# Kernel tuning notes

Hardware: AMD Instinct MI355X
Metric: run time of the kernel (lower is better)

The kernel has to match this reference:

```python
import jax, jax.numpy as jnp
import numpy as np

PHI = 0.1  # fraction of pruned weights randomized per inference


def setup_inputs() -> dict:
    key = jax.random.key(0)
    k1, k2, k3 = jax.random.split(key, 3)
    d_out, d_in, batch = 8192, 8192, 256
    W = jax.random.normal(k1, (d_out, d_in), jnp.float32) * 0.02
    prune = jax.random.uniform(k2, (d_out, d_in)) < 0.9
    W = jnp.where(prune, 0.0, W)
    mask = (W == 0.0)  # _register_masks: pruned positions
    x = jax.random.normal(k3, (batch, d_in), jnp.float32)
    return {"x": x, "W": W, "mask": mask}


def reference(x, W, mask):
    # --- _apply_random_flip (vectorized) ---
    n_pruned = int(np.asarray(jnp.sum(mask)))          # concrete mask -> static count
    n_flip = max(1, int(PHI * n_pruned))
    keep = ~mask
    n_keep = jnp.sum(keep).astype(W.dtype)
    wk = jnp.where(keep, W, 0.0)
    mean = jnp.sum(wk) / n_keep
    # torch .std() is unbiased (n-1 denominator)
    var = jnp.sum(jnp.where(keep, (W - mean) ** 2, 0.0)) / (n_keep - 1.0)
    std = jnp.sqrt(var)
    key = jax.random.key(42)
    ks, kv = jax.random.split(key)
    # uniform random permutation of pruned indices -> top_k of random scores
    scores = jnp.where(mask.ravel(), jax.random.uniform(ks, (W.size,)), -1.0)
    _, flip_idx = jax.lax.top_k(scores, n_flip)        # [n_flip] flat indices into W
    vals = jax.random.normal(kv, (n_flip,), W.dtype) * std * 0.1
    W_flipped = W.ravel().at[flip_idx].set(vals).reshape(W.shape)
    # --- base_model forward (Linear, no bias) ---
    out = x @ W_flipped.T                               # [batch, d_out]
    # --- _restore_masks: zero flipped weights again (no effect on out) ---
    _ = jnp.where(mask, 0.0, W_flipped)
    return out
```

## Files before the change

### kernel.cpp

```cpp
#include <hip/hip_runtime.h>

typedef unsigned int u32;
typedef unsigned long long u64;
typedef unsigned short u16;

#define NTOT   67108864u
#define T0P    7399424u
#define PBASE  14452u
#define NSUP   1932u
#define NWSEG  4096u
#define WCAP   2176u
#define RCAP   4352u
#define KSPLIT 4

struct Scalars {
  double sumW;
  double sumW2;
  u64 npruned;
  u64 nflip;
  float stdf;
  float pad;
};

#define OFF_COLSUM 0ull
#define OFF_ALLOC  8192ull
#define OFF_SBASE  16384ull
#define OFF_SC     24576ull
#define OFF_SEGCNT 24704ull
#define OFF_BHIST  41216ull
#define OFF_BDEST  2138368ull
#define OFF_XBF    4235520ull
#define OFF_SEGS   8429824ull
#define OFF_ROUTED 44081408ull

__host__ __device__ inline void tf2x32(u32 k0, u32 k1, u32 x0, u32 x1, u32& y0, u32& y1) {
  u32 ks2 = k0 ^ k1 ^ 0x1BD11BDAu;
  x0 += k0; x1 += k1;
#define TFR(r) { x0 += x1; x1 = (x1 << (r)) | (x1 >> (32 - (r))); x1 ^= x0; }
  TFR(13) TFR(15) TFR(26) TFR(6)  x0 += k1;  x1 += ks2 + 1u;
  TFR(17) TFR(29) TFR(16) TFR(24) x0 += ks2; x1 += k0 + 2u;
  TFR(13) TFR(15) TFR(26) TFR(6)  x0 += k0;  x1 += k1 + 3u;
  TFR(17) TFR(29) TFR(16) TFR(24) x0 += k1;  x1 += ks2 + 4u;
  TFR(13) TFR(15) TFR(26) TFR(6)  x0 += ks2; x1 += k0 + 5u;
#undef TFR
  y0 = x0; y1 = x1;
}

__device__ inline u32 jax_bits32(u32 k0, u32 k1, u32 i) {
  u32 y0, y1; tf2x32(k0, k1, 0u, i, y0, y1);
  return y0 ^ y1;
}

__device__ inline u16 f2bf(float f) {
  union { float f; u32 u; } c; c.f = f;
  u32 r = ((c.u >> 16) & 1u) + 0x7FFFu;
  return (u16)((c.u + r) >> 16);
}

__device__ inline float erfinv32(float x) {
  float w = -log1pf(-x * x);
  float p;
  if (w < 5.0f) {
    w -= 2.5f;
    p = 2.81022636e-08f;
    p = fmaf(p, w, 3.43273939e-07f);
    p = fmaf(p, w, -3.5233877e-06f);
    p = fmaf(p, w, -4.39150654e-06f);
    p = fmaf(p, w, 0.00021858087f);
    p = fmaf(p, w, -0.00125372503f);
    p = fmaf(p, w, -0.00417768164f);
    p = fmaf(p, w, 0.246640727f);
    p = fmaf(p, w, 1.50140941f);
  } else {
    w = sqrtf(w) - 3.0f;
    p = -0.000200214257f;
    p = fmaf(p, w, 0.000100950558f);
    p = fmaf(p, w, 0.00134934322f);
    p = fmaf(p, w, -0.00367342844f);
    p = fmaf(p, w, 0.00573950773f);
    p = fmaf(p, w, -0.0076224613f);
    p = fmaf(p, w, 0.00943887047f);
    p = fmaf(p, w, 1.00167406f);
    p = fmaf(p, w, 2.83297682f);
  }
  return p * x;
}

__global__ __launch_bounds__(256) void k_pass1(const float* __restrict__ W, Scalars* sc,
                                               u32* segcnt, u32* segs, u32 uk0, u32 uk1) {
  u32 t = threadIdx.x;
  u32 gid = blockIdx.x * 256 + t;
  u32 lane = t & 63;
  u32 wid = gid >> 6;
  u32* wseg = segs + (u64)wid * WCAP;
  u32 wbase = 0;
  double s = 0.0, s2 = 0.0; u32 cnt = 0;
  const u32 stride4 = 1024u * 256u * 4u;
  for (u32 b4 = gid * 4; b4 < NTOT; b4 += stride4) {
    float4 w4 = *(const float4*)(W + b4);
    u32 sb0 = jax_bits32(uk0, uk1, b4 + 0) >> 9;
    u32 sb1 = jax_bits32(uk0, uk1, b4 + 1) >> 9;
    u32 sb2 = jax_bits32(uk0, uk1, b4 + 2) >> 9;
    u32 sb3 = jax_bits32(uk0, uk1, b4 + 3) >> 9;
    float we[4] = {w4.x, w4.y, w4.z, w4.w};
    u32 sbv[4] = {sb0, sb1, sb2, sb3};
    u32 cand[4]; u32 nc = 0;
#pragma unroll
    for (int e = 0; e < 4; e++) {
      float w = we[e];
      s  += (double)w;
      s2 += (double)w * (double)w;
      bool pr = (w == 0.0f);
      cnt += pr ? 1u : 0u;
      if (pr && sbv[e] >= T0P) { cand[nc] = b4 + e; nc++; }
    }
    u32 inc = nc;
#pragma unroll
    for (int o = 1; o < 64; o <<= 1) { u32 v = (u32)__shfl_up((int)inc, o); if (lane >= (u32)o) inc += v; }
    u32 tot = (u32)__shfl((int)inc, 63);
    u32 pos = wbase + inc - nc;
    for (u32 k2 = 0; k2 < nc; k2++)
      if (pos + k2 < WCAP) wseg[pos + k2] = cand[k2];
    wbase += tot;
  }
  for (int o = 32; o > 0; o >>= 1) {
    s += __shfl_down(s, o); s2 += __shfl_down(s2, o); cnt += __shfl_down(cnt, o);
  }
  if (lane == 0) {
    atomicAdd(&sc->sumW, s);
    atomicAdd(&sc->sumW2, s2);
    atomicAdd(&sc->npruned, (u64)cnt);
    segcnt[wid] = (wbase > WCAP) ? WCAP : wbase;
  }
}

__global__ __launch_bounds__(256) void k_route_a(const u32* __restrict__ segs,
                                                 const u32* __restrict__ segcnt,
                                                 u32* bhist, u32 uk0, u32 uk1) {
  __shared__ u32 lhist[2048];
  u32 t = threadIdx.x;
  for (u32 j = t; j < 2048; j += 256) lhist[j] = 0;
  __syncthreads();
#pragma unroll 1
  for (int sg = 0; sg < 16; sg++) {
    u32 wid = blockIdx.x * 16 + sg;
    u32 n = segcnt[wid]; if (n > WCAP) n = WCAP;
    const u32* sp = segs + (u64)wid * WCAP;
    for (u32 i = t; i < n; i += 256) {
      u32 sup = (jax_bits32(uk0, uk1, sp[i]) >> 18) - PBASE;
      atomicAdd(&lhist[sup], 1u);
    }
  }
  __syncthreads();
  for (u32 j = t; j < 2048; j += 256) bhist[blockIdx.x * 2048 + j] = lhist[j];
}

__global__ __launch_bounds__(256) void k_colscan(const u32* __restrict__ bhist,
                                                 u32* bdest, u32* colsum) {
  __shared__ u32 wtmp[4];
  u32 s = blockIdx.x, t = threadIdx.x, lane = t & 63, wv = t >> 6;
  u32 v = bhist[t * 2048 + s];
  u32 inc = v;
#pragma unroll
  for (int o = 1; o < 64; o <<= 1) { u32 x = (u32)__shfl_up((int)inc, o); if (lane >= (u32)o) inc += x; }
  if (lane == 63) wtmp[wv] = inc;
  __syncthreads();
  u32 woff = 0;
  for (u32 w = 0; w < wv; w++) woff += wtmp[w];
  bdest[t * 2048 + s] = woff + inc - v;
  if (t == 255) colsum[s] = woff + inc;
}

__global__ __launch_bounds__(256) void k_scan(const u32* __restrict__ colsum, Scalars* sc,
                                              u32* alloc, u32* sbase) {
  __shared__ u32 h[2048];
  __shared__ u32 wtmp[4];
  u32 t = threadIdx.x, lane = t & 63, wv = t >> 6;
  for (u32 j = t; j < 2048; j += 256) h[j] = colsum[j];
  __syncthreads();
  {
    u32 a[8]; u32 s8 = 0;
#pragma unroll
    for (int k = 0; k < 8; k++) { a[k] = h[t * 8 + k]; s8 += a[k]; }
    u32 inc = s8;
#pragma unroll
    for (int o = 1; o < 64; o <<= 1) { u32 v = (u32)__shfl_up((int)inc, o); if (lane >= (u32)o) inc += v; }
    if (lane == 63) wtmp[wv] = inc;
    __syncthreads();
    u32 woff = 0; for (u32 w = 0; w < wv; w++) woff += wtmp[w];
    u32 base = woff + inc - s8;
#pragma unroll
    for (int k = 0; k < 8; k++) { alloc[t * 8 + k] = base; base += a[k]; }
    __syncthreads();
  }
  {
    u32 a[8]; u32 s8 = 0;
#pragma unroll
    for (int k = 0; k < 8; k++) { a[k] = h[2047 - (t * 8 + k)]; s8 += a[k]; }
    u32 inc = s8;
#pragma unroll
    for (int o = 1; o < 64; o <<= 1) { u32 v = (u32)__shfl_up((int)inc, o); if (lane >= (u32)o) inc += v; }
    if (lane == 63) wtmp[wv] = inc;
    __syncthreads();
    u32 woff = 0; for (u32 w = 0; w < wv; w++) woff += wtmp[w];
    u32 base = woff + inc - s8;
#pragma unroll
    for (int k = 0; k < 8; k++) { sbase[2047 - (t * 8 + k)] = base; base += a[k]; }
  }
  if (t == 0) {
    double nk = (double)NTOT - (double)sc->npruned;
    double mean = sc->sumW / nk;
    double var = (sc->sumW2 - 2.0 * mean * sc->sumW + nk * mean * mean) / (nk - 1.0);
    sc->stdf = (float)sqrt(var);
    u64 nfi = (u64)(0.1 * (double)sc->npruned);
    if (nfi < 1) nfi = 1;
    sc->nflip = nfi;
  }
}

__global__ __launch_bounds__(256) void k_route_b(const u32* __restrict__ segs,
                                                 const u32* __restrict__ segcnt,
                                                 const u32* __restrict__ alloc,
                                                 const u32* __restrict__ bdest,
                                                 u32* routed, u32 uk0, u32 uk1) {
  __shared__ u32 lcur[2048];
  u32 t = threadIdx.x;
  for (u32 j = t; j < 2048; j += 256) lcur[j] = alloc[j] + bdest[blockIdx.x * 2048 + j];
  __syncthreads();
#pragma unroll 1
  for (int sg = 0; sg < 16; sg++) {
    u32 wid = blockIdx.x * 16 + sg;
    u32 n = segcnt[wid]; if (n > WCAP) n = WCAP;
    const u32* sp = segs + (u64)wid * WCAP;
    for (u32 i = t; i < n; i += 256) {
      u32 idx = sp[i];
      u32 sup = (jax_bits32(uk0, uk1, idx) >> 18) - PBASE;
      u32 pos = atomicAdd(&lcur[sup], 1u);
      routed[pos] = idx;
    }
  }
}

__device__ inline void suf512(const u32* cnt, u32* suf, u32* wtmp) {
  u32 t = threadIdx.x, lane = t & 63, wv = t >> 6;
  u32 a0 = cnt[511 - t * 2], a1 = cnt[510 - t * 2];
  u32 s = a0 + a1;
  u32 inc = s;
#pragma unroll
  for (int o = 1; o < 64; o <<= 1) { u32 v = (u32)__shfl_up((int)inc, o); if (lane >= (u32)o) inc += v; }
  if (lane == 63) wtmp[wv] = inc;
  __syncthreads();
  u32 woff = 0;
  for (u32 w = 0; w < wv; w++) woff += wtmp[w];
  u32 base = woff + inc - s;
  suf[511 - t * 2] = base;
  suf[510 - t * 2] = base + a0;
  __syncthreads();
}

__global__ __launch_bounds__(256) void k_rank(float* __restrict__ W,
                                              const u32* __restrict__ colsum,
                                              const u32* __restrict__ alloc,
                                              const u32* __restrict__ sbase,
                                              const u32* __restrict__ routed,
                                              const Scalars* __restrict__ sc,
                                              u32 uk0, u32 uk1, u32 vk0, u32 vk1) {
  u32 p = blockIdx.x;
  u32 n = colsum[p]; if (n == 0) return;
  if (n > RCAP) n = RCAP;
  u64 nflip = sc->nflip;
  u32 rbase = sbase[p];
  if ((u64)rbase >= nflip) return;
  __shared__ u32 sIdx[RCAP];
  __shared__ u16 sFine[RCAP];
  __shared__ u32 pIdx[RCAP];
  __shared__ u32 hist[512], gbase[512], cur[512], wtmp[4];
  u32 t = threadIdx.x;
  for (u32 j = t; j < 512; j += 256) hist[j] = 0;
  __syncthreads();
  const u32* src = routed + alloc[p];
  for (u32 i = t; i < n; i += 256) {
    u32 idx = src[i];
    u32 f = (jax_bits32(uk0, uk1, idx) >> 9) & 511u;
    sIdx[i] = idx;
    sFine[i] = (u16)f;
    atomicAdd(&hist[f], 1u);
  }
  __syncthreads();
  suf512(hist, gbase, wtmp);
  for (u32 j = t; j < 512; j += 256) cur[j] = gbase[j];
  __syncthreads();
  for (u32 i = t; i < n; i += 256) {
    u32 pos = atomicAdd(&cur[sFine[i]], 1u);
    pIdx[pos] = sIdx[i];
  }
  __syncthreads();
  float stdf = sc->stdf;
  for (u32 i = t; i < n; i += 256) {
    u32 f = sFine[i];
    u32 g0 = gbase[f], g1 = g0 + hist[f];
    u32 v = sIdx[i];
    u32 ord = 0;
    for (u32 q = g0; q < g1; q++) ord += (pIdx[q] < v) ? 1u : 0u;
    u64 rank = (u64)rbase + g0 + ord;
    if (rank >= nflip) continue;
    u32 bits = jax_bits32(vk0, vk1, (u32)rank);
    union { u32 u; float fl; } cv; cv.u = 0x3F800000u | (bits >> 9);
    float fu = cv.fl - 1.0f;
    const float lo = -0.99999994f;
    float u2 = fmaxf(lo, fu * 2.0f + lo);
    float nrm = 1.41421354f * erfinv32(u2);
    W[v] = (nrm * stdf) * 0.1f;
  }
}

__global__ __launch_bounds__(256) void k_xconv(const float* __restrict__ x, u16* __restrict__ xbf) {
  u32 i = blockIdx.x * blockDim.x + threadIdx.x;
  float4 v = ((const float4*)x)[i];
  ushort4 o; o.x = f2bf(v.x); o.y = f2bf(v.y); o.z = f2bf(v.z); o.w = f2bf(v.w);
  ((ushort4*)xbf)[i] = o;
}

typedef __bf16 bf16x8 __attribute__((ext_vector_type(8)));
typedef float f32x4 __attribute__((ext_vector_type(4)));

__global__ __launch_bounds__(256, 2) void k_gemm(const u16* __restrict__ xbf,
                                                 const float* __restrict__ W,
                                                 float* __restrict__ out) {
  __shared__ u16 xs[256 * 72];
  __shared__ u16 wsm[64 * 72];
  u32 tid = threadIdx.x;
  u32 lane = tid & 63, wv = tid >> 6;
  u32 nt0 = blockIdx.x * 64;
  u32 kbase = blockIdx.y * (8192 / KSPLIT);
  f32x4 acc[4][4];
#pragma unroll
  for (int i = 0; i < 4; i++)
#pragma unroll
    for (int j = 0; j < 4; j++) acc[i][j] = (f32x4){0.f, 0.f, 0.f, 0.f};

  for (u32 kb = kbase; kb < kbase + 2048u; kb += 64u) {
#pragma unroll
    for (int r8 = 0; r8 < 8; r8++) {
      u32 row = r8 * 32 + (tid >> 3);
      u32 kseg = (tid & 7) * 8;
      uint4 v = *(const uint4*)(xbf + (u64)row * 8192 + kb + kseg);
      *(uint4*)&xs[row * 72 + kseg] = v;
    }
#pragma unroll
    for (int r = 0; r < 4; r++) {
      u32 f4 = r * 256 + tid;
      u32 row = f4 >> 4;
      u32 kc = (f4 & 15) * 4;
      float4 v = *(const float4*)(W + (u64)(nt0 + row) * 8192 + kb + kc);
      ushort4 o; o.x = f2bf(v.x); o.y = f2bf(v.y); o.z = f2bf(v.z); o.w = f2bf(v.w);
      *(ushort4*)&wsm[row * 72 + kc] = o;
    }
    __syncthreads();
#pragma unroll
    for (int ks = 0; ks < 2; ks++) {
      bf16x8 a[4], b[4];
      u32 koff = ks * 32 + (lane >> 4) * 8;
      u32 rsel = lane & 15;
#pragma unroll
      for (int mt = 0; mt < 4; mt++) a[mt] = *(bf16x8*)&xs[(wv * 64 + mt * 16 + rsel) * 72 + koff];
#pragma unroll
      for (int nt = 0; nt < 4; nt++) b[nt] = *(bf16x8*)&wsm[(nt * 16 + rsel) * 72 + koff];
#pragma unroll
      for (int mt = 0; mt < 4; mt++)
#pragma unroll
        for (int nt = 0; nt < 4; nt++)
          acc[mt][nt] = __builtin_amdgcn_mfma_f32_16x16x32_bf16(a[mt], b[nt], acc[mt][nt], 0, 0, 0);
    }
    __syncthreads();
  }
  u32 quad = lane >> 4, col = lane & 15;
#pragma unroll
  for (int mt = 0; mt < 4; mt++)
#pragma unroll
    for (int nt = 0; nt < 4; nt++) {
      u32 n = nt0 + nt * 16 + col;
#pragma unroll
      for (int rg = 0; rg < 4; rg++) {
        u32 m = wv * 64 + mt * 16 + quad * 4 + rg;
        atomicAdd(&out[(u64)m * 8192 + n], acc[mt][nt][rg]);
      }
    }
}

extern "C" void kernel_launch(void* const* d_in, const int* in_sizes, int n_in,
                              void* d_out, int out_size, void* d_ws, size_t ws_size,
                              hipStream_t stream) {
  const float* x; float* W;
  if (in_sizes[0] == 2097152) { x = (const float*)d_in[0]; W = (float*)d_in[1]; }
  else                        { x = (const float*)d_in[1]; W = (float*)d_in[0]; }
  float* out = (float*)d_out;
  char* ws = (char*)d_ws;

  u32* colsum = (u32*)(ws + OFF_COLSUM);
  u32* alloc  = (u32*)(ws + OFF_ALLOC);
  u32* sbase  = (u32*)(ws + OFF_SBASE);
  Scalars* sc = (Scalars*)(ws + OFF_SC);
  u32* segcnt = (u32*)(ws + OFF_SEGCNT);
  u32* bhist  = (u32*)(ws + OFF_BHIST);
  u32* bdest  = (u32*)(ws + OFF_BDEST);
  u16* xbf    = (u16*)(ws + OFF_XBF);
  u32* segs   = (u32*)(ws + OFF_SEGS);
  u32* routed = (u32*)(ws + OFF_ROUTED);

  u32 a0, a1, b0, b1;
  tf2x32(0u, 42u, 0u, 0u, a0, a1);
  tf2x32(0u, 42u, 0u, 1u, b0, b1);

  hipMemsetAsync(sc, 0, sizeof(Scalars), stream);
  hipMemsetAsync(out, 0, (size_t)out_size * 4, stream);

  k_xconv<<<2048, 256, 0, stream>>>(x, xbf);
  k_pass1<<<1024, 256, 0, stream>>>(W, sc, segcnt, segs, a0, a1);
  k_route_a<<<256, 256, 0, stream>>>(segs, segcnt, bhist, a0, a1);
  k_colscan<<<2048, 256, 0, stream>>>(bhist, bdest, colsum);
  k_scan<<<1, 256, 0, stream>>>(colsum, sc, alloc, sbase);
  k_route_b<<<256, 256, 0, stream>>>(segs, segcnt, alloc, bdest, routed, a0, a1);
  k_rank<<<NSUP, 256, 0, stream>>>(W, colsum, alloc, sbase, routed, sc, a0, a1, b0, b1);
  dim3 g(128, KSPLIT);
  k_gemm<<<g, 256, 0, stream>>>(xbf, W, out);
}
```

Measured before the change: 1.022 ms.

## Fuse histogram into pass1, prestage W as bf16, stop mutating input W

Pass1 now also writes a bf16 copy of W and builds the per-block superbucket histogram in shared memory, which removes the separate route_a kernel and its recomputation of random bits. The rank kernel writes flipped values into the bf16 copy, so the input W is no longer modified, and the GEMM loads bf16 W directly, halving its W traffic and dropping per-tile conversions. Histograms and offsets are stored as u16 with 8 histogram rows per colscan thread. The cost is an extra 128MB bf16 write in pass1, and the u16 counts could overflow if candidate counts were larger.

```diff
diff --git a/kernel.cpp b/kernel.cpp
--- a/kernel.cpp
+++ b/kernel.cpp
@@ -8,8 +8,9 @@
 #define T0P    7399424u
 #define PBASE  14452u
 #define NSUP   1932u
-#define NWSEG  4096u
-#define WCAP   2176u
+#define NBLK   2048u
+#define NWSEG  8192u
+#define WCAP   1152u
 #define RCAP   4352u
 #define KSPLIT 4
 
@@ -26,12 +27,13 @@
 #define OFF_ALLOC  8192ull
 #define OFF_SBASE  16384ull
 #define OFF_SC     24576ull
-#define OFF_SEGCNT 24704ull
-#define OFF_BHIST  41216ull
-#define OFF_BDEST  2138368ull
-#define OFF_XBF    4235520ull
-#define OFF_SEGS   8429824ull
-#define OFF_ROUTED 44081408ull
+#define OFF_SEGCNT 24832ull
+#define OFF_BHIST  57600ull
+#define OFF_BDEST  8446208ull
+#define OFF_XBF    16834816ull
+#define OFF_WBF    21029120ull
+#define OFF_SEGS   155246848ull
+#define OFF_ROUTED 192995584ull
 
 __host__ __device__ inline void tf2x32(u32 k0, u32 k1, u32 x0, u32 x1, u32& y0, u32& y1) {
   u32 ks2 = k0 ^ k1 ^ 0x1BD11BDAu;
@@ -87,7 +89,11 @@
 }
 
 __global__ __launch_bounds__(256) void k_pass1(const float* __restrict__ W, Scalars* sc,
-                                               u32* segcnt, u32* segs, u32 uk0, u32 uk1) {
+                                               u32* segcnt, u32* segs, u16* bhist,
+                                               u16* wbf, u32 uk0, u32 uk1) {
+  __shared__ u32 lhist[2048];
+  for (u32 j = threadIdx.x; j < 2048; j += 256) lhist[j] = 0;
+  __syncthreads();
   u32 t = threadIdx.x;
   u32 gid = blockIdx.x * 256 + t;
   u32 lane = t & 63;
@@ -95,24 +101,29 @@
   u32* wseg = segs + (u64)wid * WCAP;
   u32 wbase = 0;
   double s = 0.0, s2 = 0.0; u32 cnt = 0;
-  const u32 stride4 = 1024u * 256u * 4u;
-  for (u32 b4 = gid * 4; b4 < NTOT; b4 += stride4) {
-    float4 w4 = *(const float4*)(W + b4);
-    u32 sb0 = jax_bits32(uk0, uk1, b4 + 0) >> 9;
-    u32 sb1 = jax_bits32(uk0, uk1, b4 + 1) >> 9;
-    u32 sb2 = jax_bits32(uk0, uk1, b4 + 2) >> 9;
-    u32 sb3 = jax_bits32(uk0, uk1, b4 + 3) >> 9;
-    float we[4] = {w4.x, w4.y, w4.z, w4.w};
-    u32 sbv[4] = {sb0, sb1, sb2, sb3};
-    u32 cand[4]; u32 nc = 0;
-#pragma unroll
-    for (int e = 0; e < 4; e++) {
-      float w = we[e];
-      s  += (double)w;
-      s2 += (double)w * (double)w;
-      bool pr = (w == 0.0f);
+  const u32 stride8 = NBLK * 256u * 8u;
+  for (u32 b8 = gid * 8; b8 < NTOT; b8 += stride8) {
+    float4 wa = *(const float4*)(W + b8);
+    float4 wb = *(const float4*)(W + b8 + 4);
+    u32 sb[8];
+#pragma unroll
+    for (int e = 0; e < 8; e++) sb[e] = jax_bits32(uk0, uk1, b8 + e) >> 9;
+    float we[8] = {wa.x, wa.y, wa.z, wa.w, wb.x, wb.y, wb.z, wb.w};
+    ushort4 o1, o2;
+    o1.x = f2bf(wa.x); o1.y = f2bf(wa.y); o1.z = f2bf(wa.z); o1.w = f2bf(wa.w);
+    o2.x = f2bf(wb.x); o2.y = f2bf(wb.y); o2.z = f2bf(wb.z); o2.w = f2bf(wb.w);
+    *(ushort4*)(wbf + b8) = o1;
+    *(ushort4*)(wbf + b8 + 4) = o2;
+    float cs  = ((wa.x + wa.y) + (wa.z + wa.w)) + ((wb.x + wb.y) + (wb.z + wb.w));
+    float cs2 = ((wa.x * wa.x + wa.y * wa.y) + (wa.z * wa.z + wa.w * wa.w)) +
+                ((wb.x * wb.x + wb.y * wb.y) + (wb.z * wb.z + wb.w * wb.w));
+    s += (double)cs; s2 += (double)cs2;
+    u32 candI[8], candS[8]; u32 nc = 0;
+#pragma unroll
+    for (int e = 0; e < 8; e++) {
+      bool pr = (we[e] == 0.0f);
       cnt += pr ? 1u : 0u;
-      if (pr && sbv[e] >= T0P) { cand[nc] = b4 + e; nc++; }
+      if (pr && sb[e] >= T0P) { candI[nc] = b8 + e; candS[nc] = (sb[e] >> 9) - PBASE; nc++; }
     }
     u32 inc = nc;
 #pragma unroll
@@ -120,7 +131,7 @@
     u32 tot = (u32)__shfl((int)inc, 63);
     u32 pos = wbase + inc - nc;
     for (u32 k2 = 0; k2 < nc; k2++)
-      if (pos + k2 < WCAP) wseg[pos + k2] = cand[k2];
+      if (pos + k2 < WCAP) { wseg[pos + k2] = candI[k2]; atomicAdd(&lhist[candS[k2]], 1u); }
     wbase += tot;
   }
   for (int o = 32; o > 0; o >>= 1) {
@@ -132,43 +143,28 @@
     atomicAdd(&sc->npruned, (u64)cnt);
     segcnt[wid] = (wbase > WCAP) ? WCAP : wbase;
   }
-}
-
-__global__ __launch_bounds__(256) void k_route_a(const u32* __restrict__ segs,
-                                                 const u32* __restrict__ segcnt,
-                                                 u32* bhist, u32 uk0, u32 uk1) {
-  __shared__ u32 lhist[2048];
-  u32 t = threadIdx.x;
-  for (u32 j = t; j < 2048; j += 256) lhist[j] = 0;
-  __syncthreads();
-#pragma unroll 1
-  for (int sg = 0; sg < 16; sg++) {
-    u32 wid = blockIdx.x * 16 + sg;
-    u32 n = segcnt[wid]; if (n > WCAP) n = WCAP;
-    const u32* sp = segs + (u64)wid * WCAP;
-    for (u32 i = t; i < n; i += 256) {
-      u32 sup = (jax_bits32(uk0, uk1, sp[i]) >> 18) - PBASE;
-      atomicAdd(&lhist[sup], 1u);
-    }
-  }
-  __syncthreads();
-  for (u32 j = t; j < 2048; j += 256) bhist[blockIdx.x * 2048 + j] = lhist[j];
-}
-
-__global__ __launch_bounds__(256) void k_colscan(const u32* __restrict__ bhist,
-                                                 u32* bdest, u32* colsum) {
+  __syncthreads();
+  for (u32 j = t; j < 2048; j += 256) bhist[blockIdx.x * 2048 + j] = (u16)lhist[j];
+}
+
+__global__ __launch_bounds__(256) void k_colscan(const u16* __restrict__ bhist,
+                                                 u16* bdest, u32* colsum) {
   __shared__ u32 wtmp[4];
   u32 s = blockIdx.x, t = threadIdx.x, lane = t & 63, wv = t >> 6;
-  u32 v = bhist[t * 2048 + s];
-  u32 inc = v;
-#pragma unroll
-  for (int o = 1; o < 64; o <<= 1) { u32 x = (u32)__shfl_up((int)inc, o); if (lane >= (u32)o) inc += x; }
+  u32 a[8]; u32 s8 = 0;
+#pragma unroll
+  for (int k = 0; k < 8; k++) { a[k] = bhist[(t * 8 + k) * 2048 + s]; s8 += a[k]; }
+  u32 inc = s8;
+#pragma unroll
+  for (int o = 1; o < 64; o <<= 1) { u32 v = (u32)__shfl_up((int)inc, o); if (lane >= (u32)o) inc += v; }
   if (lane == 63) wtmp[wv] = inc;
   __syncthreads();
   u32 woff = 0;
   for (u32 w = 0; w < wv; w++) woff += wtmp[w];
-  bdest[t * 2048 + s] = woff + inc - v;
-  if (t == 255) colsum[s] = woff + inc;
+  u32 base = woff + inc - s8;
+#pragma unroll
+  for (int k = 0; k < 8; k++) { bdest[(t * 8 + k) * 2048 + s] = (u16)base; base += a[k]; }
+  if (t == 255) colsum[s] = base;
 }
 
 __global__ __launch_bounds__(256) void k_scan(const u32* __restrict__ colsum, Scalars* sc,
@@ -218,18 +214,19 @@
   }
 }
 
-__global__ __launch_bounds__(256) void k_route_b(const u32* __restrict__ segs,
-                                                 const u32* __restrict__ segcnt,
-                                                 const u32* __restrict__ alloc,
-                                                 const u32* __restrict__ bdest,
-                                                 u32* routed, u32 uk0, u32 uk1) {
+__global__ __launch_bounds__(256) void k_route(const u32* __restrict__ segs,
+                                               const u32* __restrict__ segcnt,
+                                               const u32* __restrict__ alloc,
+                                               const u16* __restrict__ bdest,
+                                               u32* routed, u32 uk0, u32 uk1) {
   __shared__ u32 lcur[2048];
   u32 t = threadIdx.x;
-  for (u32 j = t; j < 2048; j += 256) lcur[j] = alloc[j] + bdest[blockIdx.x * 2048 + j];
+  for (u32 j = t; j < 2048; j += 256)
+    lcur[j] = alloc[j] + (u32)bdest[(blockIdx.x * 8) * 2048 + j];
   __syncthreads();
 #pragma unroll 1
-  for (int sg = 0; sg < 16; sg++) {
-    u32 wid = blockIdx.x * 16 + sg;
+  for (int sg = 0; sg < 32; sg++) {
+    u32 wid = blockIdx.x * 32 + sg;
     u32 n = segcnt[wid]; if (n > WCAP) n = WCAP;
     const u32* sp = segs + (u64)wid * WCAP;
     for (u32 i = t; i < n; i += 256) {
@@ -258,7 +255,7 @@
   __syncthreads();
 }
 
-__global__ __launch_bounds__(256) void k_rank(float* __restrict__ W,
+__global__ __launch_bounds__(256) void k_rank(u16* __restrict__ wbf,
                                               const u32* __restrict__ colsum,
                                               const u32* __restrict__ alloc,
                                               const u32* __restrict__ sbase,
@@ -310,7 +307,7 @@
     const float lo = -0.99999994f;
     float u2 = fmaxf(lo, fu * 2.0f + lo);
     float nrm = 1.41421354f * erfinv32(u2);
-    W[v] = (nrm * stdf) * 0.1f;
+    wbf[v] = f2bf((nrm * stdf) * 0.1f);
   }
 }
 
@@ -325,7 +322,7 @@
 typedef float f32x4 __attribute__((ext_vector_type(4)));
 
 __global__ __launch_bounds__(256, 2) void k_gemm(const u16* __restrict__ xbf,
-                                                 const float* __restrict__ W,
+                                                 const u16* __restrict__ wbf,
                                                  float* __restrict__ out) {
   __shared__ u16 xs[256 * 72];
   __shared__ u16 wsm[64 * 72];
@@ -348,13 +345,12 @@
       *(uint4*)&xs[row * 72 + kseg] = v;
     }
 #pragma unroll
-    for (int r = 0; r < 4; r++) {
-      u32 f4 = r * 256 + tid;
-      u32 row = f4 >> 4;
-      u32 kc = (f4 & 15) * 4;
-      float4 v = *(const float4*)(W + (u64)(nt0 + row) * 8192 + kb + kc);
-      ushort4 o; o.x = f2bf(v.x); o.y = f2bf(v.y); o.z = f2bf(v.z); o.w = f2bf(v.w);
-      *(ushort4*)&wsm[row * 72 + kc] = o;
+    for (int r = 0; r < 2; r++) {
+      u32 c = r * 256 + tid;
+      u32 row = c >> 3;
+      u32 kseg = (c & 7) * 8;
+      uint4 v = *(const uint4*)(wbf + (u64)(nt0 + row) * 8192 + kb + kseg);
+      *(uint4*)&wsm[row * 72 + kseg] = v;
     }
     __syncthreads();
 #pragma unroll
@@ -391,9 +387,9 @@
 extern "C" void kernel_launch(void* const* d_in, const int* in_sizes, int n_in,
                               void* d_out, int out_size, void* d_ws, size_t ws_size,
                               hipStream_t stream) {
-  const float* x; float* W;
-  if (in_sizes[0] == 2097152) { x = (const float*)d_in[0]; W = (float*)d_in[1]; }
-  else                        { x = (const float*)d_in[1]; W = (float*)d_in[0]; }
+  const float* x; const float* W;
+  if (in_sizes[0] == 2097152) { x = (const float*)d_in[0]; W = (const float*)d_in[1]; }
+  else                        { x = (const float*)d_in[1]; W = (const float*)d_in[0]; }
   float* out = (float*)d_out;
   char* ws = (char*)d_ws;
 
@@ -402,9 +398,10 @@
   u32* sbase  = (u32*)(ws + OFF_SBASE);
   Scalars* sc = (Scalars*)(ws + OFF_SC);
   u32* segcnt = (u32*)(ws + OFF_SEGCNT);
-  u32* bhist  = (u32*)(ws + OFF_BHIST);
-  u32* bdest  = (u32*)(ws + OFF_BDEST);
+  u16* bhist  = (u16*)(ws + OFF_BHIST);
+  u16* bdest  = (u16*)(ws + OFF_BDEST);
   u16* xbf    = (u16*)(ws + OFF_XBF);
+  u16* wbf    = (u16*)(ws + OFF_WBF);
   u32* segs   = (u32*)(ws + OFF_SEGS);
   u32* routed = (u32*)(ws + OFF_ROUTED);
 
@@ -416,12 +413,11 @@
   hipMemsetAsync(out, 0, (size_t)out_size * 4, stream);
 
   k_xconv<<<2048, 256, 0, stream>>>(x, xbf);
-  k_pass1<<<1024, 256, 0, stream>>>(W, sc, segcnt, segs, a0, a1);
-  k_route_a<<<256, 256, 0, stream>>>(segs, segcnt, bhist, a0, a1);
+  k_pass1<<<NBLK, 256, 0, stream>>>(W, sc, segcnt, segs, bhist, wbf, a0, a1);
   k_colscan<<<2048, 256, 0, stream>>>(bhist, bdest, colsum);
   k_scan<<<1, 256, 0, stream>>>(colsum, sc, alloc, sbase);
-  k_route_b<<<256, 256, 0, stream>>>(segs, segcnt, alloc, bdest, routed, a0, a1);
-  k_rank<<<NSUP, 256, 0, stream>>>(W, colsum, alloc, sbase, routed, sc, a0, a1, b0, b1);
+  k_route<<<256, 256, 0, stream>>>(segs, segcnt, alloc, bdest, routed, a0, a1);
+  k_rank<<<NSUP, 256, 0, stream>>>(wbf, colsum, alloc, sbase, routed, sc, a0, a1, b0, b1);
   dim3 g(128, KSPLIT);
-  k_gemm<<<g, 256, 0, stream>>>(xbf, W, out);
-}
+  k_gemm<<<g, 256, 0, stream>>>(xbf, wbf, out);
+}
```

New measurement: 1.151 ms. 1.13x slower.

## Bucket flipped-weight writes by address before scattering into W, narrow route histograms

Applied to the files above, without the earlier changes.

Instead of k_rank scattering random-normal values directly into W at random addresses, it now writes (value,index) pairs in rank order. Two new kernels bucket these pairs by 32K-element address block and then apply them block by block, so the writes into W land in localized regions. The change also doubles the pass1 grid, halves the per-wave segment capacity, and stores the per-block histograms and destinations as u16 to shrink their traffic. The cost is two extra launches, extra workspace traffic for the pairs, and possible silent drops if a bucket exceeds CAPB or a segment exceeds WCAP.

```diff
diff --git a/kernel.cpp b/kernel.cpp
--- a/kernel.cpp
+++ b/kernel.cpp
@@ -8,9 +8,10 @@
 #define T0P    7399424u
 #define PBASE  14452u
 #define NSUP   1932u
-#define NWSEG  4096u
-#define WCAP   2176u
+#define NBLK   2048u
+#define WCAP   1152u
 #define RCAP   4352u
+#define CAPB   3328u
 #define KSPLIT 4
 
 struct Scalars {
@@ -27,11 +28,14 @@
 #define OFF_SBASE  16384ull
 #define OFF_SC     24576ull
 #define OFF_SEGCNT 24704ull
-#define OFF_BHIST  41216ull
-#define OFF_BDEST  2138368ull
-#define OFF_XBF    4235520ull
-#define OFF_SEGS   8429824ull
-#define OFF_ROUTED 44081408ull
+#define OFF_ACUR   57472ull
+#define OFF_BHIST  188544ull
+#define OFF_BDEST  1237120ull
+#define OFF_XBF    2285696ull
+#define OFF_SEGS   6480000ull
+#define OFF_ROUTED 44228736ull
+#define OFF_WPAIRS 74637440ull
+#define OFF_PAIRS2 126637440ull
 
 __host__ __device__ inline void tf2x32(u32 k0, u32 k1, u32 x0, u32 x1, u32& y0, u32& y1) {
   u32 ks2 = k0 ^ k1 ^ 0x1BD11BDAu;
@@ -95,7 +99,7 @@
   u32* wseg = segs + (u64)wid * WCAP;
   u32 wbase = 0;
   double s = 0.0, s2 = 0.0; u32 cnt = 0;
-  const u32 stride4 = 1024u * 256u * 4u;
+  const u32 stride4 = NBLK * 256u * 4u;
   for (u32 b4 = gid * 4; b4 < NTOT; b4 += stride4) {
     float4 w4 = *(const float4*)(W + b4);
     u32 sb0 = jax_bits32(uk0, uk1, b4 + 0) >> 9;
@@ -136,14 +140,14 @@
 
 __global__ __launch_bounds__(256) void k_route_a(const u32* __restrict__ segs,
                                                  const u32* __restrict__ segcnt,
-                                                 u32* bhist, u32 uk0, u32 uk1) {
+                                                 u16* bhist, u32 uk0, u32 uk1) {
   __shared__ u32 lhist[2048];
   u32 t = threadIdx.x;
   for (u32 j = t; j < 2048; j += 256) lhist[j] = 0;
   __syncthreads();
 #pragma unroll 1
-  for (int sg = 0; sg < 16; sg++) {
-    u32 wid = blockIdx.x * 16 + sg;
+  for (int sg = 0; sg < 32; sg++) {
+    u32 wid = blockIdx.x * 32 + sg;
     u32 n = segcnt[wid]; if (n > WCAP) n = WCAP;
     const u32* sp = segs + (u64)wid * WCAP;
     for (u32 i = t; i < n; i += 256) {
@@ -152,14 +156,14 @@
     }
   }
   __syncthreads();
-  for (u32 j = t; j < 2048; j += 256) bhist[blockIdx.x * 2048 + j] = lhist[j];
-}
-
-__global__ __launch_bounds__(256) void k_colscan(const u32* __restrict__ bhist,
-                                                 u32* bdest, u32* colsum) {
+  for (u32 j = t; j < 2048; j += 256) bhist[blockIdx.x * 2048 + j] = (u16)lhist[j];
+}
+
+__global__ __launch_bounds__(256) void k_colscan(const u16* __restrict__ bhist,
+                                                 u16* bdest, u32* colsum) {
   __shared__ u32 wtmp[4];
   u32 s = blockIdx.x, t = threadIdx.x, lane = t & 63, wv = t >> 6;
-  u32 v = bhist[t * 2048 + s];
+  u32 v = (u32)bhist[t * 2048 + s];
   u32 inc = v;
 #pragma unroll
   for (int o = 1; o < 64; o <<= 1) { u32 x = (u32)__shfl_up((int)inc, o); if (lane >= (u32)o) inc += x; }
@@ -167,7 +171,7 @@
   __syncthreads();
   u32 woff = 0;
   for (u32 w = 0; w < wv; w++) woff += wtmp[w];
-  bdest[t * 2048 + s] = woff + inc - v;
+  bdest[t * 2048 + s] = (u16)(woff + inc - v);
   if (t == 255) colsum[s] = woff + inc;
 }
 
@@ -221,15 +225,16 @@
 __global__ __launch_bounds__(256) void k_route_b(const u32* __restrict__ segs,
                                                  const u32* __restrict__ segcnt,
                                                  const u32* __restrict__ alloc,
-                                                 const u32* __restrict__ bdest,
+                                                 const u16* __restrict__ bdest,
                                                  u32* routed, u32 uk0, u32 uk1) {
   __shared__ u32 lcur[2048];
   u32 t = threadIdx.x;
-  for (u32 j = t; j < 2048; j += 256) lcur[j] = alloc[j] + bdest[blockIdx.x * 2048 + j];
+  for (u32 j = t; j < 2048; j += 256)
+    lcur[j] = alloc[j] + (u32)bdest[blockIdx.x * 2048 + j];
   __syncthreads();
 #pragma unroll 1
-  for (int sg = 0; sg < 16; sg++) {
-    u32 wid = blockIdx.x * 16 + sg;
+  for (int sg = 0; sg < 32; sg++) {
+    u32 wid = blockIdx.x * 32 + sg;
     u32 n = segcnt[wid]; if (n > WCAP) n = WCAP;
     const u32* sp = segs + (u64)wid * WCAP;
     for (u32 i = t; i < n; i += 256) {
@@ -258,7 +263,7 @@
   __syncthreads();
 }
 
-__global__ __launch_bounds__(256) void k_rank(float* __restrict__ W,
+__global__ __launch_bounds__(256) void k_rank(u64* __restrict__ wpairs,
                                               const u32* __restrict__ colsum,
                                               const u32* __restrict__ alloc,
                                               const u32* __restrict__ sbase,
@@ -310,7 +315,36 @@
     const float lo = -0.99999994f;
     float u2 = fmaxf(lo, fu * 2.0f + lo);
     float nrm = 1.41421354f * erfinv32(u2);
-    W[v] = (nrm * stdf) * 0.1f;
+    union { float fl; u32 u; } vb; vb.fl = (nrm * stdf) * 0.1f;
+    wpairs[rank] = ((u64)vb.u << 32) | v;
+  }
+}
+
+__global__ __launch_bounds__(256) void k_aroute(const u64* __restrict__ wpairs,
+                                                const Scalars* __restrict__ sc,
+                                                u32* acur, u64* pairs2) {
+  u64 nflip = sc->nflip;
+  u64 chunk = (nflip + 511) >> 9;
+  u64 beg = (u64)blockIdx.x * chunk;
+  u64 end = beg + chunk; if (end > nflip) end = nflip;
+  for (u64 i = beg + threadIdx.x; i < end; i += 256) {
+    u64 pr = wpairs[i];
+    u32 bk = ((u32)pr) >> 15;
+    u32 pos = atomicAdd(&acur[bk * 16], 1u);
+    if (pos < CAPB) pairs2[(u64)bk * CAPB + pos] = pr;
+  }
+}
+
+__global__ __launch_bounds__(256) void k_apply(float* __restrict__ W,
+                                               const u32* __restrict__ acur,
+                                               const u64* __restrict__ pairs2) {
+  u32 b = blockIdx.x;
+  u32 n = acur[b * 16]; if (n > CAPB) n = CAPB;
+  const u64* p = pairs2 + (u64)b * CAPB;
+  for (u32 i = threadIdx.x; i < n; i += 256) {
+    u64 pr = p[i];
+    union { u32 u; float fl; } vb; vb.u = (u32)(pr >> 32);
+    W[(u32)pr] = vb.fl;
   }
 }
 
@@ -402,26 +436,32 @@
   u32* sbase  = (u32*)(ws + OFF_SBASE);
   Scalars* sc = (Scalars*)(ws + OFF_SC);
   u32* segcnt = (u32*)(ws + OFF_SEGCNT);
-  u32* bhist  = (u32*)(ws + OFF_BHIST);
-  u32* bdest  = (u32*)(ws + OFF_BDEST);
+  u32* acur   = (u32*)(ws + OFF_ACUR);
+  u16* bhist  = (u16*)(ws + OFF_BHIST);
+  u16* bdest  = (u16*)(ws + OFF_BDEST);
   u16* xbf    = (u16*)(ws + OFF_XBF);
   u32* segs   = (u32*)(ws + OFF_SEGS);
   u32* routed = (u32*)(ws + OFF_ROUTED);
+  u64* wpairs = (u64*)(ws + OFF_WPAIRS);
+  u64* pairs2 = (u64*)(ws + OFF_PAIRS2);
 
   u32 a0, a1, b0, b1;
   tf2x32(0u, 42u, 0u, 0u, a0, a1);
   tf2x32(0u, 42u, 0u, 1u, b0, b1);
 
   hipMemsetAsync(sc, 0, sizeof(Scalars), stream);
+  hipMemsetAsync(acur, 0, 2048 * 16 * 4, stream);
   hipMemsetAsync(out, 0, (size_t)out_size * 4, stream);
 
   k_xconv<<<2048, 256, 0, stream>>>(x, xbf);
-  k_pass1<<<1024, 256, 0, stream>>>(W, sc, segcnt, segs, a0, a1);
+  k_pass1<<<NBLK, 256, 0, stream>>>(W, sc, segcnt, segs, a0, a1);
   k_route_a<<<256, 256, 0, stream>>>(segs, segcnt, bhist, a0, a1);
   k_colscan<<<2048, 256, 0, stream>>>(bhist, bdest, colsum);
   k_scan<<<1, 256, 0, stream>>>(colsum, sc, alloc, sbase);
   k_route_b<<<256, 256, 0, stream>>>(segs, segcnt, alloc, bdest, routed, a0, a1);
-  k_rank<<<NSUP, 256, 0, stream>>>(W, colsum, alloc, sbase, routed, sc, a0, a1, b0, b1);
+  k_rank<<<NSUP, 256, 0, stream>>>(wpairs, colsum, alloc, sbase, routed, sc, a0, a1, b0, b1);
+  k_aroute<<<512, 256, 0, stream>>>(wpairs, sc, acur, pairs2);
+  k_apply<<<2048, 256, 0, stream>>>(W, acur, pairs2);
   dim3 g(128, KSPLIT);
   k_gemm<<<g, 256, 0, stream>>>(xbf, W, out);
 }
```

Measured after the change: 1.640 ms. 60.5% more time.

## Quadruple pass1 grid, tighten candidate threshold, shrink histograms to u16, halve GEMM K-split

Applied to the files above, without the earlier changes.

The pass1 scan now runs on 4096 blocks, each thread handling 8 elements per iteration, so there are four times as many per-wave segments, each with a smaller capacity. The candidate threshold is raised so fewer pruned indices are routed and ranked, and the superbucket count drops to match. Per-block histograms and destination offsets are stored as u16 to cut workspace traffic, and the GEMM K-split goes from 4 to 2 to halve atomic output accumulation. The tighter threshold and smaller segment capacity carry a risk of overflow or of missing top-k candidates if the counts do not hold.

```diff
diff --git a/kernel.cpp b/kernel.cpp
--- a/kernel.cpp
+++ b/kernel.cpp
@@ -5,13 +5,14 @@
 typedef unsigned short u16;
 
 #define NTOT   67108864u
-#define T0P    7399424u
-#define PBASE  14452u
-#define NSUP   1932u
-#define NWSEG  4096u
-#define WCAP   2176u
+#define T0P    7533568u
+#define PBASE  14714u
+#define NSUP   1670u
+#define NBLK   4096u
+#define NWSEG  16384u
+#define WCAP   640u
 #define RCAP   4352u
-#define KSPLIT 4
+#define KSPLIT 2
 
 struct Scalars {
   double sumW;
@@ -27,11 +28,11 @@
 #define OFF_SBASE  16384ull
 #define OFF_SC     24576ull
 #define OFF_SEGCNT 24704ull
-#define OFF_BHIST  41216ull
-#define OFF_BDEST  2138368ull
-#define OFF_XBF    4235520ull
-#define OFF_SEGS   8429824ull
-#define OFF_ROUTED 44081408ull
+#define OFF_BHIST  90240ull
+#define OFF_BDEST  1138816ull
+#define OFF_XBF    2187392ull
+#define OFF_SEGS   6381696ull
+#define OFF_ROUTED 48324736ull
 
 __host__ __device__ inline void tf2x32(u32 k0, u32 k1, u32 x0, u32 x1, u32& y0, u32& y1) {
   u32 ks2 = k0 ^ k1 ^ 0x1BD11BDAu;
@@ -95,24 +96,23 @@
   u32* wseg = segs + (u64)wid * WCAP;
   u32 wbase = 0;
   double s = 0.0, s2 = 0.0; u32 cnt = 0;
-  const u32 stride4 = 1024u * 256u * 4u;
-  for (u32 b4 = gid * 4; b4 < NTOT; b4 += stride4) {
-    float4 w4 = *(const float4*)(W + b4);
-    u32 sb0 = jax_bits32(uk0, uk1, b4 + 0) >> 9;
-    u32 sb1 = jax_bits32(uk0, uk1, b4 + 1) >> 9;
-    u32 sb2 = jax_bits32(uk0, uk1, b4 + 2) >> 9;
-    u32 sb3 = jax_bits32(uk0, uk1, b4 + 3) >> 9;
-    float we[4] = {w4.x, w4.y, w4.z, w4.w};
-    u32 sbv[4] = {sb0, sb1, sb2, sb3};
-    u32 cand[4]; u32 nc = 0;
-#pragma unroll
-    for (int e = 0; e < 4; e++) {
+  const u32 stride8 = NBLK * 256u * 8u;
+  for (u32 b8 = gid * 8; b8 < NTOT; b8 += stride8) {
+    float4 wa = *(const float4*)(W + b8);
+    float4 wb = *(const float4*)(W + b8 + 4);
+    u32 sb[8];
+#pragma unroll
+    for (int e = 0; e < 8; e++) sb[e] = jax_bits32(uk0, uk1, b8 + e) >> 9;
+    float we[8] = {wa.x, wa.y, wa.z, wa.w, wb.x, wb.y, wb.z, wb.w};
+    u32 cand[8]; u32 nc = 0;
+#pragma unroll
+    for (int e = 0; e < 8; e++) {
       float w = we[e];
       s  += (double)w;
       s2 += (double)w * (double)w;
       bool pr = (w == 0.0f);
       cnt += pr ? 1u : 0u;
-      if (pr && sbv[e] >= T0P) { cand[nc] = b4 + e; nc++; }
+      if (pr && sb[e] >= T0P) { cand[nc] = b8 + e; nc++; }
     }
     u32 inc = nc;
 #pragma unroll
@@ -136,14 +136,14 @@
 
 __global__ __launch_bounds__(256) void k_route_a(const u32* __restrict__ segs,
                                                  const u32* __restrict__ segcnt,
-                                                 u32* bhist, u32 uk0, u32 uk1) {
+                                                 u16* bhist, u32 uk0, u32 uk1) {
   __shared__ u32 lhist[2048];
   u32 t = threadIdx.x;
   for (u32 j = t; j < 2048; j += 256) lhist[j] = 0;
   __syncthreads();
 #pragma unroll 1
-  for (int sg = 0; sg < 16; sg++) {
-    u32 wid = blockIdx.x * 16 + sg;
+  for (int sg = 0; sg < 64; sg++) {
+    u32 wid = blockIdx.x * 64 + sg;
     u32 n = segcnt[wid]; if (n > WCAP) n = WCAP;
     const u32* sp = segs + (u64)wid * WCAP;
     for (u32 i = t; i < n; i += 256) {
@@ -152,14 +152,14 @@
     }
   }
   __syncthreads();
-  for (u32 j = t; j < 2048; j += 256) bhist[blockIdx.x * 2048 + j] = lhist[j];
-}
-
-__global__ __launch_bounds__(256) void k_colscan(const u32* __restrict__ bhist,
-                                                 u32* bdest, u32* colsum) {
+  for (u32 j = t; j < 2048; j += 256) bhist[blockIdx.x * 2048 + j] = (u16)lhist[j];
+}
+
+__global__ __launch_bounds__(256) void k_colscan(const u16* __restrict__ bhist,
+                                                 u16* bdest, u32* colsum) {
   __shared__ u32 wtmp[4];
   u32 s = blockIdx.x, t = threadIdx.x, lane = t & 63, wv = t >> 6;
-  u32 v = bhist[t * 2048 + s];
+  u32 v = (u32)bhist[t * 2048 + s];
   u32 inc = v;
 #pragma unroll
   for (int o = 1; o < 64; o <<= 1) { u32 x = (u32)__shfl_up((int)inc, o); if (lane >= (u32)o) inc += x; }
@@ -167,7 +167,7 @@
   __syncthreads();
   u32 woff = 0;
   for (u32 w = 0; w < wv; w++) woff += wtmp[w];
-  bdest[t * 2048 + s] = woff + inc - v;
+  bdest[t * 2048 + s] = (u16)(woff + inc - v);
   if (t == 255) colsum[s] = woff + inc;
 }
 
@@ -221,15 +221,16 @@
 __global__ __launch_bounds__(256) void k_route_b(const u32* __restrict__ segs,
                                                  const u32* __restrict__ segcnt,
                                                  const u32* __restrict__ alloc,
-                                                 const u32* __restrict__ bdest,
+                                                 const u16* __restrict__ bdest,
                                                  u32* routed, u32 uk0, u32 uk1) {
   __shared__ u32 lcur[2048];
   u32 t = threadIdx.x;
-  for (u32 j = t; j < 2048; j += 256) lcur[j] = alloc[j] + bdest[blockIdx.x * 2048 + j];
+  for (u32 j = t; j < 2048; j += 256)
+    lcur[j] = alloc[j] + (u32)bdest[blockIdx.x * 2048 + j];
   __syncthreads();
 #pragma unroll 1
-  for (int sg = 0; sg < 16; sg++) {
-    u32 wid = blockIdx.x * 16 + sg;
+  for (int sg = 0; sg < 64; sg++) {
+    u32 wid = blockIdx.x * 64 + sg;
     u32 n = segcnt[wid]; if (n > WCAP) n = WCAP;
     const u32* sp = segs + (u64)wid * WCAP;
     for (u32 i = t; i < n; i += 256) {
@@ -339,7 +340,7 @@
 #pragma unroll
     for (int j = 0; j < 4; j++) acc[i][j] = (f32x4){0.f, 0.f, 0.f, 0.f};
 
-  for (u32 kb = kbase; kb < kbase + 2048u; kb += 64u) {
+  for (u32 kb = kbase; kb < kbase + (8192u / KSPLIT); kb += 64u) {
 #pragma unroll
     for (int r8 = 0; r8 < 8; r8++) {
       u32 row = r8 * 32 + (tid >> 3);
@@ -402,8 +403,8 @@
   u32* sbase  = (u32*)(ws + OFF_SBASE);
   Scalars* sc = (Scalars*)(ws + OFF_SC);
   u32* segcnt = (u32*)(ws + OFF_SEGCNT);
-  u32* bhist  = (u32*)(ws + OFF_BHIST);
-  u32* bdest  = (u32*)(ws + OFF_BDEST);
+  u16* bhist  = (u16*)(ws + OFF_BHIST);
+  u16* bdest  = (u16*)(ws + OFF_BDEST);
   u16* xbf    = (u16*)(ws + OFF_XBF);
   u32* segs   = (u32*)(ws + OFF_SEGS);
   u32* routed = (u32*)(ws + OFF_ROUTED);
@@ -416,7 +417,7 @@
   hipMemsetAsync(out, 0, (size_t)out_size * 4, stream);
 
   k_xconv<<<2048, 256, 0, stream>>>(x, xbf);
-  k_pass1<<<1024, 256, 0, stream>>>(W, sc, segcnt, segs, a0, a1);
+  k_pass1<<<NBLK, 256, 0, stream>>>(W, sc, segcnt, segs, a0, a1);
   k_route_a<<<256, 256, 0, stream>>>(segs, segcnt, bhist, a0, a1);
   k_colscan<<<2048, 256, 0, stream>>>(bhist, bdest, colsum);
   k_scan<<<1, 256, 0, stream>>>(colsum, sc, alloc, sbase);
```

New measurement: 1.422 ms. +39.1%, slower.
